# Performance work log

Measured on AMD Instinct MI355X. Metric: run time of the kernel, lower is better.

Reference implementation:

```python
import jax, jax.numpy as jnp
import numpy as np

D = 1024  # embed dim == mlp hidden dim (hiddendim=input_dim in source)

def _layernorm(x, gamma, beta, eps=1e-5):
    mu = jnp.mean(x, axis=-1, keepdims=True)
    var = jnp.var(x, axis=-1, keepdims=True)
    return (x - mu) * jax.lax.rsqrt(var + eps) * gamma + beta

def setup_inputs() -> dict:
    key = jax.random.key(0)
    ks = jax.random.split(key, 16)
    B, N = 16, 1024
    s = 1.0 / np.sqrt(D)
    inp = {
        "x": jax.random.normal(ks[0], (B, N, D), jnp.float32),
        "ln1_g": jnp.ones((D,), jnp.float32),
        "ln1_b": jnp.zeros((D,), jnp.float32),
        "ln2_g": jnp.ones((D,), jnp.float32),
        "ln2_b": jnp.zeros((D,), jnp.float32),
        "wq": jax.random.normal(ks[1], (D, D), jnp.float32) * s,
        "bq": jnp.zeros((D,), jnp.float32),
        "wk": jax.random.normal(ks[2], (D, D), jnp.float32) * s,
        "bk": jnp.zeros((D,), jnp.float32),
        "wv": jax.random.normal(ks[3], (D, D), jnp.float32) * s,
        "bv": jnp.zeros((D,), jnp.float32),
        "wo": jax.random.normal(ks[4], (D, D), jnp.float32) * s,
        "bo": jnp.zeros((D,), jnp.float32),
        "w1": jax.random.normal(ks[5], (D, D), jnp.float32) * s,
        "b1": jnp.zeros((D,), jnp.float32),
        "w2": jax.random.normal(ks[6], (D, D), jnp.float32) * s,
        "b2": jnp.zeros((D,), jnp.float32),
    }
    return inp

def reference(x, ln1_g, ln1_b, ln2_g, ln2_b, wq, bq, wk, bk, wv, bv, wo, bo, w1, b1, w2, b2):
    d = x.shape[-1]
    # pre-LN -> naive full-matrix attention (single head over full D, scale D**0.5)
    xn = _layernorm(x, ln1_g, ln1_b)
    q = xn @ wq + bq
    k = xn @ wk + bk
    v = xn @ wv + bv
    scores = jnp.einsum('bnd,bmd->bnm', q, k) / jnp.sqrt(jnp.asarray(d, x.dtype))
    attn = jax.nn.softmax(scores, axis=-1)  # [B,N,N] materialized, as in source
    mha = jnp.einsum('bnm,bmd->bnd', attn, v) @ wo + bo
    x_update = x + mha
    # pre-LN -> MLP: Linear->GELU->Linear->GELU, hidden == D
    xu = _layernorm(x_update, ln2_g, ln2_b)
    h = jax.nn.gelu(xu @ w1 + b1, approximate=False)
    h = jax.nn.gelu(h @ w2 + b2, approximate=False)
    return h + x_update
```

## Files before the change

kernel.cpp:

```cpp
#include <hip/hip_runtime.h>
#include <hip/hip_bf16.h>
#include <math.h>

#define BATCH 16
#define SEQ   1024
#define DIM   1024
#define ROWS  (BATCH*SEQ)
#define KD    1024
#define KTILES (KD/32)

typedef __bf16 bf16_t;
typedef __bf16 bf16x4 __attribute__((ext_vector_type(4)));
typedef __bf16 bf16x8 __attribute__((ext_vector_type(8)));
typedef float  f32x4  __attribute__((ext_vector_type(4)));

__device__ __forceinline__ float gelu_exact(float x) {
    return 0.5f * x * (1.0f + erff(x * 0.70710678118654752f));
}
__device__ __forceinline__ void split2(float v, bf16_t& h, bf16_t& l) {
    h = (bf16_t)v;
    l = (bf16_t)(v - (float)h);
}

__global__ __launch_bounds__(256)
void fill0_kernel(float* __restrict__ p, size_t n) {
    const size_t i = (size_t)blockIdx.x * blockDim.x + threadIdx.x;
    const size_t stride = (size_t)gridDim.x * blockDim.x;
    for (size_t j = i; j < n; j += stride) p[j] = 0.0f;
}

__global__ __launch_bounds__(256)
void ln_split_kernel(const float* __restrict__ x, const float* __restrict__ g,
                     const float* __restrict__ b,
                     bf16_t* __restrict__ oh, bf16_t* __restrict__ ol) {
    __shared__ float s1[4], s2[4];
    const size_t row = blockIdx.x;
    const int t = threadIdx.x;
    const float4 v = ((const float4*)(x + row * DIM))[t];
    float s  = v.x + v.y + v.z + v.w;
    float ss = v.x*v.x + v.y*v.y + v.z*v.z + v.w*v.w;
    #pragma unroll
    for (int off = 32; off > 0; off >>= 1) {
        s  += __shfl_down(s,  off, 64);
        ss += __shfl_down(ss, off, 64);
    }
    const int wid = t >> 6, lane = t & 63;
    if (lane == 0) { s1[wid] = s; s2[wid] = ss; }
    __syncthreads();
    s  = s1[0] + s1[1] + s1[2] + s1[3];
    ss = s2[0] + s2[1] + s2[2] + s2[3];
    const float mean = s * (1.0f / DIM);
    const float var  = ss * (1.0f / DIM) - mean * mean;
    const float rstd = rsqrtf(var + 1e-5f);
    const float4 gv = ((const float4*)g)[t];
    const float4 bv = ((const float4*)b)[t];
    float o[4];
    o[0] = (v.x - mean) * rstd * gv.x + bv.x;
    o[1] = (v.y - mean) * rstd * gv.y + bv.y;
    o[2] = (v.z - mean) * rstd * gv.z + bv.z;
    o[3] = (v.w - mean) * rstd * gv.w + bv.w;
    bf16x4 h, l;
    #pragma unroll
    for (int i = 0; i < 4; ++i) { bf16_t hh, ll; split2(o[i], hh, ll); h[i] = hh; l[i] = ll; }
    *(bf16x4*)&oh[row * DIM + t * 4] = h;
    *(bf16x4*)&ol[row * DIM + t * 4] = l;
}

__global__ __launch_bounds__(256)
void softmax_split_kernel(const float* __restrict__ sc,
                          bf16_t* __restrict__ ph, bf16_t* __restrict__ pl) {
    __shared__ float sm[4], ssum[4];
    const size_t row = blockIdx.x;
    const int t = threadIdx.x;
    float4 v = ((const float4*)(sc + row * SEQ))[t];
    float m = fmaxf(fmaxf(v.x, v.y), fmaxf(v.z, v.w));
    #pragma unroll
    for (int off = 32; off > 0; off >>= 1) m = fmaxf(m, __shfl_down(m, off, 64));
    const int wid = t >> 6, lane = t & 63;
    if (lane == 0) sm[wid] = m;
    __syncthreads();
    m = fmaxf(fmaxf(sm[0], sm[1]), fmaxf(sm[2], sm[3]));
    v.x = expf(v.x - m); v.y = expf(v.y - m);
    v.z = expf(v.z - m); v.w = expf(v.w - m);
    float s = v.x + v.y + v.z + v.w;
    #pragma unroll
    for (int off = 32; off > 0; off >>= 1) s += __shfl_down(s, off, 64);
    if (lane == 0) ssum[wid] = s;
    __syncthreads();
    s = ssum[0] + ssum[1] + ssum[2] + ssum[3];
    const float inv = 1.0f / s;
    float o[4] = { v.x * inv, v.y * inv, v.z * inv, v.w * inv };
    bf16x4 h, l;
    #pragma unroll
    for (int i = 0; i < 4; ++i) { bf16_t hh, ll; split2(o[i], hh, ll); h[i] = hh; l[i] = ll; }
    *(bf16x4*)&ph[row * SEQ + t * 4] = h;
    *(bf16x4*)&pl[row * SEQ + t * 4] = l;
}

__global__ __launch_bounds__(256)
void wsplit_kernel(const float* __restrict__ w,
                   bf16_t* __restrict__ oh, bf16_t* __restrict__ ol) {
    __shared__ float T[64][68];
    const int k0 = blockIdx.x * 64, n0 = blockIdx.y * 64;
    const int t = threadIdx.x;
    const int tr = t >> 4, tc = t & 15;
    #pragma unroll
    for (int j = 0; j < 4; ++j) {
        const float4 v = *(const float4*)&w[(size_t)(k0 + tr + j * 16) * DIM + n0 + tc * 4];
        *(float4*)&T[tr + j * 16][tc * 4] = v;
    }
    __syncthreads();
    #pragma unroll
    for (int j = 0; j < 4; ++j) {
        const int nl = tr + j * 16;
        const int kl = tc * 4;
        bf16x4 h, l;
        #pragma unroll
        for (int i = 0; i < 4; ++i) {
            bf16_t hh, ll; split2(T[kl + i][nl], hh, ll);
            h[i] = hh; l[i] = ll;
        }
        *(bf16x4*)&oh[(size_t)(n0 + nl) * KD + k0 + kl] = h;
        *(bf16x4*)&ol[(size_t)(n0 + nl) * KD + k0 + kl] = l;
    }
}

template<int BIAS, bool GELU, bool SPLIT, bool RES>
__global__ __launch_bounds__(256)
void gemm_mfma(const bf16_t* __restrict__ Ah, const bf16_t* __restrict__ Al,
               const bf16_t* __restrict__ Bh, const bf16_t* __restrict__ Bl,
               const float* __restrict__ bias, const float* res,
               float* Cf, bf16_t* __restrict__ Ch, bf16_t* __restrict__ Cl,
               int Nn, int ldb,
               long long sA, long long sB, long long sC, float scale) {
    __shared__ alignas(16) bf16_t LAh[128 * 32];
    __shared__ alignas(16) bf16_t LAl[128 * 32];
    __shared__ alignas(16) bf16_t LBh[128 * 32];
    __shared__ alignas(16) bf16_t LBl[128 * 32];

    const int bm0 = blockIdx.x * 128;
    const int bn0 = blockIdx.y * 128;
    const int bz  = blockIdx.z;
    Ah += (size_t)bz * sA;  Al += (size_t)bz * sA;
    Bh += (size_t)bz * sB;  Bl += (size_t)bz * sB;
    const size_t cbase = (size_t)bz * sC;

    const int tid  = threadIdx.x;
    const int lane = tid & 63;
    const int w    = tid >> 6;
    const int wm   = w >> 1, wn = w & 1;

    const int r0 = tid >> 2;
    const int g0 = tid & 3;
    const int r1 = r0 + 64;
    const bf16_t* pAh0 = Ah + (size_t)(bm0 + r0) * KD + g0 * 8;
    const bf16_t* pAh1 = pAh0 + (size_t)64 * KD;
    const bf16_t* pAl0 = Al + (size_t)(bm0 + r0) * KD + g0 * 8;
    const bf16_t* pAl1 = pAl0 + (size_t)64 * KD;
    const bf16_t* pBh0 = Bh + (size_t)(bn0 + r0) * ldb + g0 * 8;
    const bf16_t* pBh1 = pBh0 + (size_t)64 * ldb;
    const bf16_t* pBl0 = Bl + (size_t)(bn0 + r0) * ldb + g0 * 8;
    const bf16_t* pBl1 = pBl0 + (size_t)64 * ldb;
    const int lw0 = r0 * 32 + ((g0 ^ ((r0 >> 1) & 3)) * 8);
    const int lw1 = r1 * 32 + ((g0 ^ ((r1 >> 1) & 3)) * 8);

    int roffA[4], roffB[4];
    #pragma unroll
    for (int i = 0; i < 4; ++i) {
        const int ra = wm * 64 + i * 16 + (lane & 15);
        roffA[i] = ra * 32 + (((lane >> 4) ^ ((ra >> 1) & 3)) * 8);
        const int rb = wn * 64 + i * 16 + (lane & 15);
        roffB[i] = rb * 32 + (((lane >> 4) ^ ((rb >> 1) & 3)) * 8);
    }

    f32x4 acc[4][4];
    #pragma unroll
    for (int i = 0; i < 4; ++i)
        #pragma unroll
        for (int j = 0; j < 4; ++j)
            acc[i][j] = (f32x4)0.0f;

    uint4 vAh0 = *(const uint4*)pAh0, vAh1 = *(const uint4*)pAh1;
    uint4 vAl0 = *(const uint4*)pAl0, vAl1 = *(const uint4*)pAl1;
    uint4 vBh0 = *(const uint4*)pBh0, vBh1 = *(const uint4*)pBh1;
    uint4 vBl0 = *(const uint4*)pBl0, vBl1 = *(const uint4*)pBl1;

    for (int kt = 0; kt < KTILES; ++kt) {
        __syncthreads();
        *(uint4*)&LAh[lw0] = vAh0;  *(uint4*)&LAh[lw1] = vAh1;
        *(uint4*)&LAl[lw0] = vAl0;  *(uint4*)&LAl[lw1] = vAl1;
        *(uint4*)&LBh[lw0] = vBh0;  *(uint4*)&LBh[lw1] = vBh1;
        *(uint4*)&LBl[lw0] = vBl0;  *(uint4*)&LBl[lw1] = vBl1;
        __syncthreads();
        if (kt < KTILES - 1) {
            pAh0 += 32; pAh1 += 32; pAl0 += 32; pAl1 += 32;
            pBh0 += 32; pBh1 += 32; pBl0 += 32; pBl1 += 32;
            vAh0 = *(const uint4*)pAh0; vAh1 = *(const uint4*)pAh1;
            vAl0 = *(const uint4*)pAl0; vAl1 = *(const uint4*)pAl1;
            vBh0 = *(const uint4*)pBh0; vBh1 = *(const uint4*)pBh1;
            vBl0 = *(const uint4*)pBl0; vBl1 = *(const uint4*)pBl1;
        }
        bf16x8 bh[4], bl[4];
        #pragma unroll
        for (int i = 0; i < 4; ++i) {
            bh[i] = *(const bf16x8*)&LBh[roffB[i]];
            bl[i] = *(const bf16x8*)&LBl[roffB[i]];
        }
        #pragma unroll
        for (int im = 0; im < 4; ++im) {
            const bf16x8 ah = *(const bf16x8*)&LAh[roffA[im]];
            const bf16x8 al = *(const bf16x8*)&LAl[roffA[im]];
            #pragma unroll
            for (int in = 0; in < 4; ++in) {
                acc[im][in] = __builtin_amdgcn_mfma_f32_16x16x32_bf16(ah, bh[in], acc[im][in], 0, 0, 0);
                acc[im][in] = __builtin_amdgcn_mfma_f32_16x16x32_bf16(ah, bl[in], acc[im][in], 0, 0, 0);
                acc[im][in] = __builtin_amdgcn_mfma_f32_16x16x32_bf16(al, bh[in], acc[im][in], 0, 0, 0);
            }
        }
    }

    const int colb = bn0 + wn * 64 + (lane & 15);
    const int rowb = bm0 + wm * 64 + 4 * (lane >> 4);
    #pragma unroll
    for (int im = 0; im < 4; ++im) {
        #pragma unroll
        for (int in = 0; in < 4; ++in) {
            const int col = colb + in * 16;
            float bc = 0.0f;
            if (BIAS == 1) bc = bias[col];
            #pragma unroll
            for (int j = 0; j < 4; ++j) {
                const int row = rowb + im * 16 + j;
                float v = acc[im][in][j] * scale;
                if (BIAS == 1) v += bc;
                if (BIAS == 2) v += bias[row];
                if (GELU) v = gelu_exact(v);
                const size_t off = cbase + (size_t)row * Nn + col;
                if (SPLIT) {
                    bf16_t hh, ll; split2(v, hh, ll);
                    Ch[off] = hh; Cl[off] = ll;
                } else {
                    if (RES) v += res[off];
                    Cf[off] = v;
                }
            }
        }
    }
}

extern "C" void kernel_launch(void* const* d_in, const int* in_sizes, int n_in,
                              void* d_out, int out_size, void* d_ws, size_t ws_size,
                              hipStream_t stream) {
    const float* x     = (const float*)d_in[0];
    const float* ln1_g = (const float*)d_in[1];
    const float* ln1_b = (const float*)d_in[2];
    const float* ln2_g = (const float*)d_in[3];
    const float* ln2_b = (const float*)d_in[4];
    const float* wq    = (const float*)d_in[5];
    const float* bq    = (const float*)d_in[6];
    const float* wk    = (const float*)d_in[7];
    const float* bk    = (const float*)d_in[8];
    const float* wv    = (const float*)d_in[9];
    const float* bv    = (const float*)d_in[10];
    const float* wo    = (const float*)d_in[11];
    const float* bo    = (const float*)d_in[12];
    const float* w1    = (const float*)d_in[13];
    const float* b1    = (const float*)d_in[14];
    const float* w2    = (const float*)d_in[15];
    const float* b2    = (const float*)d_in[16];

    const size_t EL  = (size_t)ROWS * DIM;
    const size_t WEL = (size_t)DIM * KD;
    const size_t NEED = (6 * EL + 12 * WEL) * sizeof(bf16_t);

    if (ws_size < NEED) {
        fill0_kernel<<<2048, 256, 0, stream>>>((float*)d_out, (size_t)out_size);
        return;
    }

    bf16_t* base = (bf16_t*)d_ws;
    bf16_t* S0h = base;            bf16_t* S0l = S0h + EL;
    bf16_t* S1h = base + 2 * EL;   bf16_t* S1l = S1h + EL;
    bf16_t* S2h = base + 4 * EL;   bf16_t* S2l = S2h + EL;
    bf16_t* Wb  = base + 6 * EL;
    bf16_t* Kh  = (bf16_t*)d_out;  bf16_t* Kl = Kh + EL;
    float* sc   = (float*)S0h;
    float* xupd = (float*)S1h;

    const dim3 blk(256);
    const dim3 gw(ROWS / 128, DIM / 128, 1);
    const dim3 gvt(DIM / 128, ROWS / 128, 1);
    const dim3 ga(SEQ / 128, SEQ / 128, BATCH);
    const long long sND = (long long)SEQ * DIM;
    const long long sNN = (long long)SEQ * SEQ;

    ln_split_kernel<<<ROWS, blk, 0, stream>>>(x, ln1_g, ln1_b, S0h, S0l);
    const float* Wsrc[6] = { wq, wk, wv, wo, w1, w2 };
    bf16_t *wTh[6], *wTl[6];
    for (int i = 0; i < 6; ++i) {
        wTh[i] = Wb + (size_t)i * 2 * WEL;
        wTl[i] = wTh[i] + WEL;
        wsplit_kernel<<<dim3(16, 16), blk, 0, stream>>>(Wsrc[i], wTh[i], wTl[i]);
    }
    gemm_mfma<1, false, true, false><<<gw, blk, 0, stream>>>(
        S0h, S0l, wTh[0], wTl[0], bq, nullptr, nullptr, S1h, S1l, DIM, KD, 0, 0, 0, 1.0f);
    gemm_mfma<1, false, true, false><<<gw, blk, 0, stream>>>(
        S0h, S0l, wTh[1], wTl[1], bk, nullptr, nullptr, Kh, Kl, DIM, KD, 0, 0, 0, 1.0f);
    gemm_mfma<2, false, true, false><<<gvt, blk, 0, stream>>>(
        wTh[2], wTl[2], S0h, S0l, bv, nullptr, nullptr, S2h, S2l, ROWS, KD, 0, 0, 0, 1.0f);
    gemm_mfma<0, false, false, false><<<ga, blk, 0, stream>>>(
        S1h, S1l, Kh, Kl, nullptr, nullptr, sc, nullptr, nullptr, SEQ, KD, sND, sND, sNN, 0.03125f);
    softmax_split_kernel<<<ROWS, blk, 0, stream>>>(sc, S1h, S1l);
    gemm_mfma<0, false, true, false><<<ga, blk, 0, stream>>>(
        S1h, S1l, S2h, S2l, nullptr, nullptr, nullptr, S0h, S0l, DIM, ROWS, sNN, SEQ, sND, 1.0f);
    gemm_mfma<1, false, false, true><<<gw, blk, 0, stream>>>(
        S0h, S0l, wTh[3], wTl[3], bo, x, xupd, nullptr, nullptr, DIM, KD, 0, 0, 0, 1.0f);
    ln_split_kernel<<<ROWS, blk, 0, stream>>>(xupd, ln2_g, ln2_b, S0h, S0l);
    gemm_mfma<1, true, true, false><<<gw, blk, 0, stream>>>(
        S0h, S0l, wTh[4], wTl[4], b1, nullptr, nullptr, S2h, S2l, DIM, KD, 0, 0, 0, 1.0f);
    gemm_mfma<1, true, false, true><<<gw, blk, 0, stream>>>(
        S2h, S2l, wTh[5], wTl[5], b2, xupd, (float*)d_out, nullptr, nullptr, DIM, KD, 0, 0, 0, 1.0f);
}
```

Before: 1.339 ms.

## Load GEMM tiles directly into LDS with global_load_lds

Replaces the register-staged global-to-LDS tile copy in the split-bf16 GEMM with direct global_load_lds DMA transfers. The XOR swizzle moves from the LDS write address to the global read address. The cost it targets is the VGPR staging and ds_write instructions. In exchange it drops the software prefetch of the next k-tile, so loads no longer overlap with the MFMA work of the previous tile, and each iteration now carries two barriers.

```diff
diff --git a/kernel.cpp b/kernel.cpp
--- a/kernel.cpp
+++ b/kernel.cpp
@@ -20,6 +20,13 @@
 __device__ __forceinline__ void split2(float v, bf16_t& h, bf16_t& l) {
     h = (bf16_t)v;
     l = (bf16_t)(v - (float)h);
+}
+
+__device__ __forceinline__ void gload16(const bf16_t* g, bf16_t* l) {
+    __builtin_amdgcn_global_load_lds(
+        (const __attribute__((address_space(1))) unsigned int*)g,
+        (__attribute__((address_space(3))) unsigned int*)l,
+        16, 0, 0);
 }
 
 __global__ __launch_bounds__(256)
@@ -150,19 +157,22 @@
     const int w    = tid >> 6;
     const int wm   = w >> 1, wn = w & 1;
 
-    const int r0 = tid >> 2;
-    const int g0 = tid & 3;
-    const int r1 = r0 + 64;
-    const bf16_t* pAh0 = Ah + (size_t)(bm0 + r0) * KD + g0 * 8;
-    const bf16_t* pAh1 = pAh0 + (size_t)64 * KD;
-    const bf16_t* pAl0 = Al + (size_t)(bm0 + r0) * KD + g0 * 8;
-    const bf16_t* pAl1 = pAl0 + (size_t)64 * KD;
-    const bf16_t* pBh0 = Bh + (size_t)(bn0 + r0) * ldb + g0 * 8;
-    const bf16_t* pBh1 = pBh0 + (size_t)64 * ldb;
-    const bf16_t* pBl0 = Bl + (size_t)(bn0 + r0) * ldb + g0 * 8;
-    const bf16_t* pBl1 = pBl0 + (size_t)64 * ldb;
-    const int lw0 = r0 * 32 + ((g0 ^ ((r0 >> 1) & 3)) * 8);
-    const int lw1 = r1 * 32 + ((g0 ^ ((r1 >> 1) & 3)) * 8);
+    const int rr0 = w * 16 + (lane >> 2);
+    const int rr1 = rr0 + 64;
+    const int c   = lane & 3;
+    const int cs0 = c ^ ((rr0 >> 1) & 3);
+    const int cs1 = c ^ ((rr1 >> 1) & 3);
+    const int ldst0 = (w * 16) * 32;
+    const int ldst1 = (64 + w * 16) * 32;
+
+    const bf16_t* gAh0 = Ah + (size_t)(bm0 + rr0) * KD + cs0 * 8;
+    const bf16_t* gAh1 = Ah + (size_t)(bm0 + rr1) * KD + cs1 * 8;
+    const bf16_t* gAl0 = Al + (size_t)(bm0 + rr0) * KD + cs0 * 8;
+    const bf16_t* gAl1 = Al + (size_t)(bm0 + rr1) * KD + cs1 * 8;
+    const bf16_t* gBh0 = Bh + (size_t)(bn0 + rr0) * ldb + cs0 * 8;
+    const bf16_t* gBh1 = Bh + (size_t)(bn0 + rr1) * ldb + cs1 * 8;
+    const bf16_t* gBl0 = Bl + (size_t)(bn0 + rr0) * ldb + cs0 * 8;
+    const bf16_t* gBl1 = Bl + (size_t)(bn0 + rr1) * ldb + cs1 * 8;
 
     int roffA[4], roffB[4];
     #pragma unroll
@@ -180,26 +190,15 @@
         for (int j = 0; j < 4; ++j)
             acc[i][j] = (f32x4)0.0f;
 
-    uint4 vAh0 = *(const uint4*)pAh0, vAh1 = *(const uint4*)pAh1;
-    uint4 vAl0 = *(const uint4*)pAl0, vAl1 = *(const uint4*)pAl1;
-    uint4 vBh0 = *(const uint4*)pBh0, vBh1 = *(const uint4*)pBh1;
-    uint4 vBl0 = *(const uint4*)pBl0, vBl1 = *(const uint4*)pBl1;
-
     for (int kt = 0; kt < KTILES; ++kt) {
+        gload16(gAh0, &LAh[ldst0]);  gload16(gAh1, &LAh[ldst1]);
+        gload16(gAl0, &LAl[ldst0]);  gload16(gAl1, &LAl[ldst1]);
+        gload16(gBh0, &LBh[ldst0]);  gload16(gBh1, &LBh[ldst1]);
+        gload16(gBl0, &LBl[ldst0]);  gload16(gBl1, &LBl[ldst1]);
+        gAh0 += 32; gAh1 += 32; gAl0 += 32; gAl1 += 32;
+        gBh0 += 32; gBh1 += 32; gBl0 += 32; gBl1 += 32;
         __syncthreads();
-        *(uint4*)&LAh[lw0] = vAh0;  *(uint4*)&LAh[lw1] = vAh1;
-        *(uint4*)&LAl[lw0] = vAl0;  *(uint4*)&LAl[lw1] = vAl1;
-        *(uint4*)&LBh[lw0] = vBh0;  *(uint4*)&LBh[lw1] = vBh1;
-        *(uint4*)&LBl[lw0] = vBl0;  *(uint4*)&LBl[lw1] = vBl1;
-        __syncthreads();
-        if (kt < KTILES - 1) {
-            pAh0 += 32; pAh1 += 32; pAl0 += 32; pAl1 += 32;
-            pBh0 += 32; pBh1 += 32; pBl0 += 32; pBl1 += 32;
-            vAh0 = *(const uint4*)pAh0; vAh1 = *(const uint4*)pAh1;
-            vAl0 = *(const uint4*)pAl0; vAl1 = *(const uint4*)pAl1;
-            vBh0 = *(const uint4*)pBh0; vBh1 = *(const uint4*)pBh1;
-            vBl0 = *(const uint4*)pBl0; vBl1 = *(const uint4*)pBl1;
-        }
+
         bf16x8 bh[4], bl[4];
         #pragma unroll
         for (int i = 0; i < 4; ++i) {
@@ -217,6 +216,7 @@
                 acc[im][in] = __builtin_amdgcn_mfma_f32_16x16x32_bf16(al, bh[in], acc[im][in], 0, 0, 0);
             }
         }
+        __syncthreads();
     }
 
     const int colb = bn0 + wn * 64 + (lane & 15);
```

New measurement: 1.217 ms. -9.0%, faster.
